# Kernel tuning notes

Hardware: AMD Instinct MI355X
Metric: run time of the kernel (lower is better)

Reference implementation:

```python
import jax, jax.numpy as jnp
from jax import lax
import numpy as np

EPS = 1e-8
NUM_ROUTES = 1152  # 32 * 6 * 6
NUM_OBJ = 10
OBJ_DIM = 16
PC_CAPS = 8
PC_CH = 32


def _squash(s, axis=-1):
    sq = jnp.sum(s * s, axis=axis, keepdims=True)
    return (sq / (1.0 + sq)) * s / jnp.sqrt(sq + EPS)


def setup_inputs() -> dict:
    key = jax.random.key(0)
    ks = jax.random.split(key, 12)
    B = 512
    image = jax.random.uniform(ks[0], (B, 1, 28, 28), dtype=jnp.float32)
    label = jax.random.randint(ks[1], (B,), 0, NUM_OBJ)
    conv_w = jax.random.normal(ks[2], (256, 1, 9, 9), dtype=jnp.float32) * 0.05
    conv_b = jnp.zeros((256,), jnp.float32)
    pc_w = jax.random.normal(ks[3], (PC_CAPS, PC_CH, 256, 9, 9), dtype=jnp.float32) * 0.02
    pc_b = jnp.zeros((PC_CAPS, PC_CH), jnp.float32)
    W_route = jax.random.normal(ks[4], (NUM_ROUTES, NUM_OBJ, OBJ_DIM, PC_CAPS), dtype=jnp.float32)
    dec_w1 = jax.random.normal(ks[5], (512, NUM_OBJ * OBJ_DIM), dtype=jnp.float32) * 0.05
    dec_b1 = jnp.zeros((512,), jnp.float32)
    dec_w2 = jax.random.normal(ks[6], (1024, 512), dtype=jnp.float32) * 0.05
    dec_b2 = jnp.zeros((1024,), jnp.float32)
    dec_w3 = jax.random.normal(ks[7], (784, 1024), dtype=jnp.float32) * 0.05
    dec_b3 = jnp.zeros((784,), jnp.float32)
    return {"image": image, "label": label, "conv_w": conv_w, "conv_b": conv_b,
            "pc_w": pc_w, "pc_b": pc_b, "W_route": W_route,
            "dec_w1": dec_w1, "dec_b1": dec_b1, "dec_w2": dec_w2, "dec_b2": dec_b2,
            "dec_w3": dec_w3, "dec_b3": dec_b3}


def reference(image, label, conv_w, conv_b, pc_w, pc_b, W_route,
              dec_w1, dec_b1, dec_w2, dec_b2, dec_w3, dec_b3):
    B = image.shape[0]
    # ConvEncoder: [B,1,28,28] -> [B,256,20,20]
    x = lax.conv_general_dilated(image, conv_w, (1, 1), 'VALID',
                                 dimension_numbers=('NCHW', 'OIHW', 'NCHW'))
    x = jax.nn.relu(x + conv_b[None, :, None, None])
    # PrimaryCaps: 8 parallel convs fused into one conv with 8*32 out channels
    pw = pc_w.reshape(PC_CAPS * PC_CH, 256, 9, 9)
    u = lax.conv_general_dilated(x, pw, (2, 2), 'VALID',
                                 dimension_numbers=('NCHW', 'OIHW', 'NCHW'))
    u = u + pc_b.reshape(-1)[None, :, None, None]  # [B,256,6,6] == stack dim=1 of [B,8,32,6,6]
    # faithful torch .view: [B,8,32,6,6] row-major -> [B,1152,8]
    u = u.reshape(B, NUM_ROUTES, PC_CAPS)
    u = _squash(u, axis=-1)
    # ObjectCaps dynamic routing
    # u_hat[b,r,j,o] = sum_c W[r,j,o,c] * u[b,r,c]
    u_hat = jnp.einsum('rjoc,brc->brjo', W_route, u)  # [B,1152,10,16]
    b_ij = jnp.zeros((B, NUM_ROUTES, NUM_OBJ), u_hat.dtype)
    v = None
    for it in range(3):
        c_ij = jax.nn.softmax(b_ij, axis=2)                  # softmax over capsules j
        s_j = jnp.einsum('brj,brjo->bjo', c_ij, u_hat)       # [B,10,16]
        v = _squash(s_j, axis=-1)
        if it < 2:
            b_ij = b_ij + jnp.einsum('brjo,bjo->brj', u_hat, v)
    obj_vectors = v[..., None]  # [B,10,16,1]
    # safe_norm over dim=2, squeeze(-1)
    y_prob = jnp.sqrt(jnp.sum(v * v, axis=-1) + EPS)  # [B,10]
    # Decoder: mask by label one-hot, MLP to reconstruction
    mask = jax.nn.one_hot(label, NUM_OBJ, dtype=v.dtype)
    masked = (v * mask[:, :, None]).reshape(B, NUM_OBJ * OBJ_DIM)
    h = jax.nn.relu(masked @ dec_w1.T + dec_b1)
    h = jax.nn.relu(h @ dec_w2.T + dec_b2)
    recon = jax.nn.sigmoid(h @ dec_w3.T + dec_b3).reshape(B, 1, 28, 28)
    return obj_vectors, recon, y_prob
```

## Files before the change

kernel.cpp:

```cpp
#include <hip/hip_runtime.h>
#include <hip/hip_bf16.h>

#define EPSF 1e-8f

typedef __attribute__((ext_vector_type(8))) short short8v;
typedef __attribute__((ext_vector_type(4))) float float4v;

#define XREG 29248
#define XSLOT 7312

static __device__ __forceinline__ unsigned short f2bf_bits(float x)
{
    return __builtin_bit_cast(unsigned short, __float2bfloat16(x));
}

__global__ __launch_bounds__(256) void k_bw2(const float* __restrict__ pw,
                                             __hip_bfloat16* __restrict__ Bw2)
{
    const int oc = blockIdx.x;
    const int t = threadIdx.x;
    __shared__ unsigned short wl[20736];
    for (int i = t; i < 20736; i += 256)
        wl[i] = f2bf_bits(pw[(size_t)oc * 20736 + i]);
    __syncthreads();
    const int r16 = oc & 15, nt = (oc >> 4) & 3, wcq = oc >> 6;
    for (int e = t; e < 2592; e += 256) {
        const int kidx = e >> 5, icc = (e >> 2) & 7, slot = e & 3;
        short8v v;
        #pragma unroll
        for (int i = 0; i < 8; ++i)
            v[i] = (short)wl[(icc * 32 + slot * 8 + i) * 81 + kidx];
        const int chunk = ((kidx * 8 + icc) * 4 + wcq) * 4 + nt;
        *(short8v*)(Bw2 + (size_t)chunk * 512 + (slot * 16 + r16) * 8) = v;
    }
}

__global__ __launch_bounds__(256) void k_conv1(const float* __restrict__ img,
                                               const float* __restrict__ cw,
                                               const float* __restrict__ cb,
                                               __hip_bfloat16* __restrict__ xt)
{
    const int b = blockIdx.x;
    const int c = threadIdx.x;
    __shared__ float simg[784];
    for (int i = c; i < 784; i += 256) simg[i] = img[b * 784 + i];
    float wreg[81];
    const float* wp = cw + c * 81;
    #pragma unroll
    for (int k = 0; k < 81; ++k) wreg[k] = wp[k];
    const float bias = cb[c];
    __syncthreads();

    const int icc = c >> 5, slot = (c >> 3) & 3, ic8 = c & 7;
    char* xbase = (char*)xt + ((size_t)b * 8 + icc) * XREG + slot * XSLOT + ic8 * 2;

    for (int h = 0; h < 20; ++h) {
        for (int wg = 0; wg < 5; ++wg) {
            float acc[4] = {bias, bias, bias, bias};
            #pragma unroll
            for (int ky = 0; ky < 9; ++ky) {
                const float* rp = &simg[(h + ky) * 28 + wg * 4];
                float v[12];
                #pragma unroll
                for (int i = 0; i < 12; ++i) v[i] = rp[i];
                #pragma unroll
                for (int kx = 0; kx < 9; ++kx) {
                    const float wv = wreg[ky * 9 + kx];
                    #pragma unroll
                    for (int i = 0; i < 4; ++i)
                        acc[i] = fmaf(v[kx + i], wv, acc[i]);
                }
            }
            #pragma unroll
            for (int i = 0; i < 4; ++i) {
                int w = wg * 4 + i;
                float av = fmaxf(acc[i], 0.f);
                int pos = 23 * h + 10 * (w & 1) + (w >> 1);
                *(unsigned short*)(xbase + pos * 16) = f2bf_bits(av);
            }
        }
    }
}

__device__ __forceinline__ void stage_x(const __hip_bfloat16* __restrict__ xt,
                                        char* dst, int b0, int icc, int t)
{
    const char* base0 = (const char*)xt + ((size_t)(b0    ) * 8 + icc) * XREG;
    const char* base1 = (const char*)xt + ((size_t)(b0 + 1) * 8 + icc) * XREG;
    #pragma unroll
    for (int k = 0; k < 7; ++k) {
        const int unit = t + k * 512;
        const char* gp = (unit < 1828) ? (base0 + unit * 16)
                                       : (base1 + (unit - 1828) * 16);
        __builtin_amdgcn_global_load_lds(
            (const __attribute__((address_space(1))) unsigned int*)gp,
            (__attribute__((address_space(3))) unsigned int*)(dst + unit * 16),
            16, 0, 0);
    }
    if (t < 72) {
        const int unit = 3584 + t;
        const char* gp = base1 + (unit - 1828) * 16;
        __builtin_amdgcn_global_load_lds(
            (const __attribute__((address_space(1))) unsigned int*)gp,
            (__attribute__((address_space(3))) unsigned int*)(dst + unit * 16),
            16, 0, 0);
    }
}

__global__ __launch_bounds__(512, 1) void k_conv2(const __hip_bfloat16* __restrict__ xt,
                                                  const __hip_bfloat16* __restrict__ Bw2,
                                                  const float* __restrict__ pcb,
                                                  float* __restrict__ u)
{
    const int b0 = blockIdx.x * 2;
    const int t = threadIdx.x;
    const int lane = t & 63, wid = t >> 6;
    const int wr = wid >> 2, wc = wid & 3;
    const int r16 = lane & 15, slot = lane >> 4;

    __shared__ alignas(16) char xs[2][58496];

    int lc[3];
    #pragma unroll
    for (int mt = 0; mt < 3; ++mt) {
        int hw = mt * 16 + r16;
        if (hw >= 36) hw = 0;
        int h = hw / 6, w = hw - h * 6;
        lc[mt] = 46 * h + w;
    }
    const int abase0 = wr * XREG + slot * XSLOT;

    float4v acc[3][4];
    #pragma unroll
    for (int mt = 0; mt < 3; ++mt)
        #pragma unroll
        for (int nt = 0; nt < 4; ++nt)
            acc[mt][nt] = (float4v){0.f, 0.f, 0.f, 0.f};

    stage_x(xt, xs[0], b0, 0, t);
    __syncthreads();

    for (int icc = 0; icc < 8; ++icc) {
        const int cur = icc & 1;
        if (icc < 7) stage_x(xt, xs[cur ^ 1], b0, icc + 1, t);

        const char* xw = xs[cur];
        const __hip_bfloat16* bp = Bw2 + ((size_t)icc * 4 + wc) * 2048 + lane * 8;

        for (int ky = 0; ky < 9; ++ky) {
            const char* ap0 = xw + abase0 + (lc[0] + 23 * ky) * 16;
            const char* ap1 = xw + abase0 + (lc[1] + 23 * ky) * 16;
            const char* ap2 = xw + abase0 + (lc[2] + 23 * ky) * 16;
            const __hip_bfloat16* bk = bp + (size_t)ky * 9 * 65536;
            #pragma unroll
            for (int kx = 0; kx < 9; ++kx) {
                const int C = (10 * (kx & 1) + (kx >> 1)) * 16;
                short8v a0 = *(const short8v*)(ap0 + C);
                short8v a1 = *(const short8v*)(ap1 + C);
                short8v a2 = *(const short8v*)(ap2 + C);
                const __hip_bfloat16* bq = bk + (size_t)kx * 65536;
                short8v bv0 = *(const short8v*)(bq);
                short8v bv1 = *(const short8v*)(bq + 512);
                short8v bv2 = *(const short8v*)(bq + 1024);
                short8v bv3 = *(const short8v*)(bq + 1536);
                acc[0][0] = __builtin_amdgcn_mfma_f32_16x16x32_bf16(a0, bv0, acc[0][0], 0, 0, 0);
                acc[0][1] = __builtin_amdgcn_mfma_f32_16x16x32_bf16(a0, bv1, acc[0][1], 0, 0, 0);
                acc[0][2] = __builtin_amdgcn_mfma_f32_16x16x32_bf16(a0, bv2, acc[0][2], 0, 0, 0);
                acc[0][3] = __builtin_amdgcn_mfma_f32_16x16x32_bf16(a0, bv3, acc[0][3], 0, 0, 0);
                acc[1][0] = __builtin_amdgcn_mfma_f32_16x16x32_bf16(a1, bv0, acc[1][0], 0, 0, 0);
                acc[1][1] = __builtin_amdgcn_mfma_f32_16x16x32_bf16(a1, bv1, acc[1][1], 0, 0, 0);
                acc[1][2] = __builtin_amdgcn_mfma_f32_16x16x32_bf16(a1, bv2, acc[1][2], 0, 0, 0);
                acc[1][3] = __builtin_amdgcn_mfma_f32_16x16x32_bf16(a1, bv3, acc[1][3], 0, 0, 0);
                acc[2][0] = __builtin_amdgcn_mfma_f32_16x16x32_bf16(a2, bv0, acc[2][0], 0, 0, 0);
                acc[2][1] = __builtin_amdgcn_mfma_f32_16x16x32_bf16(a2, bv1, acc[2][1], 0, 0, 0);
                acc[2][2] = __builtin_amdgcn_mfma_f32_16x16x32_bf16(a2, bv2, acc[2][2], 0, 0, 0);
                acc[2][3] = __builtin_amdgcn_mfma_f32_16x16x32_bf16(a2, bv3, acc[2][3], 0, 0, 0);
            }
        }
        __syncthreads();
    }

    const int b = b0 + wr;
    #pragma unroll
    for (int mt = 0; mt < 3; ++mt) {
        int hwb = mt * 16 + slot * 4;
        if (hwb < 36) {
            #pragma unroll
            for (int nt = 0; nt < 4; ++nt) {
                int oc = wc * 64 + nt * 16 + r16;
                float pb = pcb[oc];
                float4v v = acc[mt][nt];
                v.x += pb; v.y += pb; v.z += pb; v.w += pb;
                *(float4v*)(u + (size_t)b * 9216 + oc * 36 + hwb) = v;
            }
        }
    }
}

__global__ void k_squash_u(float* __restrict__ u, int ngroups)
{
    int g = blockIdx.x * blockDim.x + threadIdx.x;
    if (g >= ngroups) return;
    float4v* p = (float4v*)(u + (size_t)g * 8);
    float4v a = p[0], c = p[1];
    float sq = a.x * a.x + a.y * a.y + a.z * a.z + a.w * a.w
             + c.x * c.x + c.y * c.y + c.z * c.z + c.w * c.w;
    float scale = (sq / (1.f + sq)) / sqrtf(sq + EPSF);
    a *= scale; c *= scale;
    p[0] = a; p[1] = c;
}

__global__ __launch_bounds__(256, 2) void k_route3(const float* __restrict__ u,
                                                   const float* __restrict__ W,
                                                   const float* __restrict__ vsum,
                                                   float* __restrict__ spart, int iter)
{
    const int bid = blockIdx.x;
    const int rc = bid % 144;
    const int bc = bid / 144;
    const int r0 = rc * 8;
    const int b0 = bc * 64;
    const int t = threadIdx.x;
    const int oq = t & 3;
    const int img = t >> 2;
    const int b = b0 + img;

    __shared__ alignas(16) float Wl[10240];
    __shared__ alignas(16) float ul[64 * 68];

    #pragma unroll
    for (int k = 0; k < 10; ++k) {
        int e = t + k * 256;
        int rr = e / 320, rest = e - rr * 320;
        float4v val = *(const float4v*)(W + (size_t)(r0 + rr) * 1280 + rest * 4);
        int es = e ^ ((e >> 3) & 3);
        *(float4v*)(Wl + es * 4) = val;
    }
    #pragma unroll
    for (int k = 0; k < 4; ++k) {
        int e = t + k * 256;
        int im = e >> 4, f4 = e & 15;
        float4v val = *(const float4v*)(u + (size_t)(b0 + im) * 9216 + rc * 64 + f4 * 4);
        *(float4v*)(ul + im * 68 + f4 * 4) = val;
    }
    __syncthreads();

    float4v vv[10];
    if (iter > 0) {
        #pragma unroll
        for (int j = 0; j < 10; ++j)
            vv[j] = *(const float4v*)(vsum + (size_t)b * 160 + j * 16 + oq * 4);
    }

    float4v acc[10];
    #pragma unroll
    for (int j = 0; j < 10; ++j) acc[j] = (float4v){0.f, 0.f, 0.f, 0.f};

    const float* up = ul + img * 68;

    for (int r = 0; r < 8; ++r) {
        float4v u0 = *(const float4v*)(up + r * 8);
        float4v u1 = *(const float4v*)(up + r * 8 + 4);
        float4v uh[10];
        #pragma unroll
        for (int j = 0; j < 10; ++j) {
            #pragma unroll
            for (int oo = 0; oo < 4; ++oo) {
                int un = r * 320 + j * 32 + oq * 8 + oo * 2;
                int i0 = un ^ oq;
                int i1 = i0 ^ 1;
                float4v wlo = *(const float4v*)(Wl + i0 * 4);
                float4v whi = *(const float4v*)(Wl + i1 * 4);
                uh[j][oo] = wlo.x * u0.x + wlo.y * u0.y + wlo.z * u0.z + wlo.w * u0.w
                          + whi.x * u1.x + whi.y * u1.y + whi.z * u1.z + whi.w * u1.w;
            }
        }
        if (iter > 0) {
            float q[10];
            #pragma unroll
            for (int j = 0; j < 10; ++j) {
                float qp = uh[j].x * vv[j].x + uh[j].y * vv[j].y
                         + uh[j].z * vv[j].z + uh[j].w * vv[j].w;
                qp += __shfl_xor(qp, 1);
                qp += __shfl_xor(qp, 2);
                q[j] = qp;
            }
            float mx = q[0];
            #pragma unroll
            for (int j = 1; j < 10; ++j) mx = fmaxf(mx, q[j]);
            float ssum = 0.f;
            float c[10];
            #pragma unroll
            for (int j = 0; j < 10; ++j) { c[j] = __expf(q[j] - mx); ssum += c[j]; }
            float inv = 1.f / ssum;
            #pragma unroll
            for (int j = 0; j < 10; ++j) acc[j] += (c[j] * inv) * uh[j];
        } else {
            #pragma unroll
            for (int j = 0; j < 10; ++j) acc[j] += 0.1f * uh[j];
        }
    }

    float* dst = spart + ((size_t)rc * 512 + b) * 160 + oq * 4;
    #pragma unroll
    for (int j = 0; j < 10; ++j)
        *(float4v*)(dst + j * 16) = acc[j];
}

__global__ void k_finish(const float* __restrict__ spart, float* __restrict__ vsum,
                         const int* __restrict__ label, float* __restrict__ obj,
                         float* __restrict__ yprob, float* __restrict__ masked, int iter)
{
    const int b = blockIdx.x, t = threadIdx.x;
    if (t < 160) {
        const float* sp = spart + (size_t)b * 160 + t;
        float sv = 0.f;
        #pragma unroll 8
        for (int rc = 0; rc < 144; ++rc)
            sv += sp[(size_t)rc * 81920];
        float sq = sv * sv;
        sq += __shfl_xor(sq, 1); sq += __shfl_xor(sq, 2);
        sq += __shfl_xor(sq, 4); sq += __shfl_xor(sq, 8);
        float v = sv * (sq / (1.f + sq)) / sqrtf(sq + EPSF);
        float pv = (iter > 0) ? vsum[b * 160 + t] : 0.f;
        vsum[b * 160 + t] = pv + v;
        if (iter == 2) {
            obj[b * 160 + t] = v;
            float vv = v * v;
            vv += __shfl_xor(vv, 1); vv += __shfl_xor(vv, 2);
            vv += __shfl_xor(vv, 4); vv += __shfl_xor(vv, 8);
            int j = t >> 4;
            if ((t & 15) == 0) yprob[b * 10 + j] = sqrtf(vv + EPSF);
            masked[b * 160 + t] = (label[b] == j) ? v : 0.f;
        }
    }
}

__global__ void k_mlp(const float* __restrict__ A, const float* __restrict__ Wt,
                      const float* __restrict__ bias, float* __restrict__ C,
                      int N, int K, int act)
{
    const int m0 = blockIdx.x * 32;
    const int n0 = blockIdx.y * 32;
    const int t  = threadIdx.x;
    const int tn = t & 31, tg = t >> 5;
    __shared__ float As[32][33];
    __shared__ float Ws[32][33];
    float acc[4] = {0.f, 0.f, 0.f, 0.f};
    for (int k0 = 0; k0 < K; k0 += 32) {
        __syncthreads();
        for (int idx = t; idx < 1024; idx += 256) {
            int rr = idx >> 5, kk = idx & 31;
            As[rr][kk] = A[(size_t)(m0 + rr) * K + k0 + kk];
            int n = n0 + rr;
            Ws[rr][kk] = (n < N) ? Wt[(size_t)n * K + k0 + kk] : 0.f;
        }
        __syncthreads();
        #pragma unroll 8
        for (int kk = 0; kk < 32; ++kk) {
            float bv = Ws[tn][kk];
            #pragma unroll
            for (int i = 0; i < 4; ++i)
                acc[i] += As[tg * 4 + i][kk] * bv;
        }
    }
    int n = n0 + tn;
    if (n < N) {
        float bs = bias[n];
        #pragma unroll
        for (int i = 0; i < 4; ++i) {
            float vv = acc[i] + bs;
            vv = (act == 0) ? fmaxf(vv, 0.f) : 1.f / (1.f + expf(-vv));
            C[(size_t)(m0 + tg * 4 + i) * N + n] = vv;
        }
    }
}

extern "C" void kernel_launch(void* const* d_in, const int* in_sizes, int n_in,
                              void* d_out, int out_size, void* d_ws, size_t ws_size,
                              hipStream_t stream)
{
    const float* image  = (const float*)d_in[0];
    const int*   label  = (const int*)  d_in[1];
    const float* conv_w = (const float*)d_in[2];
    const float* conv_b = (const float*)d_in[3];
    const float* pc_w   = (const float*)d_in[4];
    const float* pc_b   = (const float*)d_in[5];
    const float* Wrt    = (const float*)d_in[6];
    const float* dw1 = (const float*)d_in[7];
    const float* db1 = (const float*)d_in[8];
    const float* dw2 = (const float*)d_in[9];
    const float* db2 = (const float*)d_in[10];
    const float* dw3 = (const float*)d_in[11];
    const float* db3 = (const float*)d_in[12];
    float* out = (float*)d_out;

    char* p = (char*)d_ws;
    __hip_bfloat16* xt  = (__hip_bfloat16*)p; p += (size_t)512 * 8 * XREG;
    float* u      = (float*)p; p += 18874368;
    __hip_bfloat16* Bw2 = (__hip_bfloat16*)p; p += 10616832;
    float* vsum   = (float*)p; p += 327680;
    float* masked = (float*)p; p += 327680;
    float* h1     = (float*)p; p += 1048576;
    float* h2     = (float*)p; p += 2097152;

    float* spart = (float*)xt;

    float* obj   = out;
    float* recon = out + 81920;
    float* yprob = out + 483328;

    k_bw2<<<256, 256, 0, stream>>>(pc_w, Bw2);
    k_conv1<<<512, 256, 0, stream>>>(image, conv_w, conv_b, xt);
    k_conv2<<<256, 512, 0, stream>>>(xt, Bw2, pc_b, u);
    k_squash_u<<<2304, 256, 0, stream>>>(u, 589824);
    for (int it = 0; it < 3; ++it) {
        k_route3<<<1152, 256, 0, stream>>>(u, Wrt, vsum, spart, it);
        k_finish<<<512, 192, 0, stream>>>(spart, vsum, label, obj, yprob, masked, it);
    }
    k_mlp<<<dim3(16, 16), 256, 0, stream>>>(masked, dw1, db1, h1, 512, 160, 0);
    k_mlp<<<dim3(16, 32), 256, 0, stream>>>(h1, dw2, db2, h2, 1024, 512, 0);
    k_mlp<<<dim3(16, 25), 256, 0, stream>>>(h2, dw3, db3, recon, 784, 1024, 1);
}
```

Measured before the change: 786.3 us.

## Use one image per conv2 block and software-pipeline A/B fragment loads

The primary-caps conv kernel now has each 256-thread block handle one image instead of two, halving LDS per block so two blocks can share a CU, and the grid grows from 256 to 512 blocks. The 9x9 kernel loop is fully unrolled into a rotating register pipeline that prefetches B weight fragments three steps ahead and A fragments from LDS two steps ahead, to hide global and LDS latency behind the MFMAs. In exchange, each B weight fragment is now fetched by twice as many blocks, and the deeper register buffering raises register pressure under the two-blocks-per-CU launch bound.

```diff
diff --git a/kernel.cpp b/kernel.cpp
--- a/kernel.cpp
+++ b/kernel.cpp
@@ -12,6 +12,11 @@
 static __device__ __forceinline__ unsigned short f2bf_bits(float x)
 {
     return __builtin_bit_cast(unsigned short, __float2bfloat16(x));
+}
+
+__device__ constexpr int aoff(int k)
+{
+    return (23 * (k / 9) + 10 * ((k % 9) & 1) + ((k % 9) >> 1)) * 16;
 }
 
 __global__ __launch_bounds__(256) void k_bw2(const float* __restrict__ pw,
@@ -83,42 +88,37 @@
 }
 
 __device__ __forceinline__ void stage_x(const __hip_bfloat16* __restrict__ xt,
-                                        char* dst, int b0, int icc, int t)
-{
-    const char* base0 = (const char*)xt + ((size_t)(b0    ) * 8 + icc) * XREG;
-    const char* base1 = (const char*)xt + ((size_t)(b0 + 1) * 8 + icc) * XREG;
+                                        char* dst, int b, int icc, int t)
+{
+    const char* base = (const char*)xt + ((size_t)b * 8 + icc) * XREG;
     #pragma unroll
     for (int k = 0; k < 7; ++k) {
-        const int unit = t + k * 512;
-        const char* gp = (unit < 1828) ? (base0 + unit * 16)
-                                       : (base1 + (unit - 1828) * 16);
+        const int unit = t + k * 256;
         __builtin_amdgcn_global_load_lds(
-            (const __attribute__((address_space(1))) unsigned int*)gp,
+            (const __attribute__((address_space(1))) unsigned int*)(base + unit * 16),
             (__attribute__((address_space(3))) unsigned int*)(dst + unit * 16),
             16, 0, 0);
     }
-    if (t < 72) {
-        const int unit = 3584 + t;
-        const char* gp = base1 + (unit - 1828) * 16;
+    if (t < 36) {
+        const int unit = 1792 + t;
         __builtin_amdgcn_global_load_lds(
-            (const __attribute__((address_space(1))) unsigned int*)gp,
+            (const __attribute__((address_space(1))) unsigned int*)(base + unit * 16),
             (__attribute__((address_space(3))) unsigned int*)(dst + unit * 16),
             16, 0, 0);
     }
 }
 
-__global__ __launch_bounds__(512, 1) void k_conv2(const __hip_bfloat16* __restrict__ xt,
+__global__ __launch_bounds__(256, 2) void k_conv2(const __hip_bfloat16* __restrict__ xt,
                                                   const __hip_bfloat16* __restrict__ Bw2,
                                                   const float* __restrict__ pcb,
                                                   float* __restrict__ u)
 {
-    const int b0 = blockIdx.x * 2;
+    const int b = blockIdx.x;
     const int t = threadIdx.x;
-    const int lane = t & 63, wid = t >> 6;
-    const int wr = wid >> 2, wc = wid & 3;
+    const int lane = t & 63, wc = t >> 6;
     const int r16 = lane & 15, slot = lane >> 4;
 
-    __shared__ alignas(16) char xs[2][58496];
+    __shared__ alignas(16) char xs[2][29248];
 
     int lc[3];
     #pragma unroll
@@ -128,7 +128,7 @@
         int h = hw / 6, w = hw - h * 6;
         lc[mt] = 46 * h + w;
     }
-    const int abase0 = wr * XREG + slot * XSLOT;
+    const int abase0 = slot * XSLOT;
 
     float4v acc[3][4];
     #pragma unroll
@@ -137,50 +137,69 @@
         for (int nt = 0; nt < 4; ++nt)
             acc[mt][nt] = (float4v){0.f, 0.f, 0.f, 0.f};
 
-    stage_x(xt, xs[0], b0, 0, t);
+    stage_x(xt, xs[0], b, 0, t);
     __syncthreads();
 
     for (int icc = 0; icc < 8; ++icc) {
         const int cur = icc & 1;
-        if (icc < 7) stage_x(xt, xs[cur ^ 1], b0, icc + 1, t);
+        if (icc < 7) stage_x(xt, xs[cur ^ 1], b, icc + 1, t);
 
         const char* xw = xs[cur];
+        const char* apm0 = xw + abase0 + lc[0] * 16;
+        const char* apm1 = xw + abase0 + lc[1] * 16;
+        const char* apm2 = xw + abase0 + lc[2] * 16;
         const __hip_bfloat16* bp = Bw2 + ((size_t)icc * 4 + wc) * 2048 + lane * 8;
 
+        short8v a[3][3];
+        short8v bv[4][4];
+        #pragma unroll
+        for (int pk = 0; pk < 2; ++pk) {
+            const int off = aoff(pk);
+            a[pk][0] = *(const short8v*)(apm0 + off);
+            a[pk][1] = *(const short8v*)(apm1 + off);
+            a[pk][2] = *(const short8v*)(apm2 + off);
+        }
+        #pragma unroll
+        for (int pk = 0; pk < 3; ++pk) {
+            const __hip_bfloat16* bq = bp + (size_t)pk * 65536;
+            bv[pk][0] = *(const short8v*)(bq);
+            bv[pk][1] = *(const short8v*)(bq + 512);
+            bv[pk][2] = *(const short8v*)(bq + 1024);
+            bv[pk][3] = *(const short8v*)(bq + 1536);
+        }
+
+        #pragma unroll
         for (int ky = 0; ky < 9; ++ky) {
-            const char* ap0 = xw + abase0 + (lc[0] + 23 * ky) * 16;
-            const char* ap1 = xw + abase0 + (lc[1] + 23 * ky) * 16;
-            const char* ap2 = xw + abase0 + (lc[2] + 23 * ky) * 16;
-            const __hip_bfloat16* bk = bp + (size_t)ky * 9 * 65536;
             #pragma unroll
             for (int kx = 0; kx < 9; ++kx) {
-                const int C = (10 * (kx & 1) + (kx >> 1)) * 16;
-                short8v a0 = *(const short8v*)(ap0 + C);
-                short8v a1 = *(const short8v*)(ap1 + C);
-                short8v a2 = *(const short8v*)(ap2 + C);
-                const __hip_bfloat16* bq = bk + (size_t)kx * 65536;
-                short8v bv0 = *(const short8v*)(bq);
-                short8v bv1 = *(const short8v*)(bq + 512);
-                short8v bv2 = *(const short8v*)(bq + 1024);
-                short8v bv3 = *(const short8v*)(bq + 1536);
-                acc[0][0] = __builtin_amdgcn_mfma_f32_16x16x32_bf16(a0, bv0, acc[0][0], 0, 0, 0);
-                acc[0][1] = __builtin_amdgcn_mfma_f32_16x16x32_bf16(a0, bv1, acc[0][1], 0, 0, 0);
-                acc[0][2] = __builtin_amdgcn_mfma_f32_16x16x32_bf16(a0, bv2, acc[0][2], 0, 0, 0);
-                acc[0][3] = __builtin_amdgcn_mfma_f32_16x16x32_bf16(a0, bv3, acc[0][3], 0, 0, 0);
-                acc[1][0] = __builtin_amdgcn_mfma_f32_16x16x32_bf16(a1, bv0, acc[1][0], 0, 0, 0);
-                acc[1][1] = __builtin_amdgcn_mfma_f32_16x16x32_bf16(a1, bv1, acc[1][1], 0, 0, 0);
-                acc[1][2] = __builtin_amdgcn_mfma_f32_16x16x32_bf16(a1, bv2, acc[1][2], 0, 0, 0);
-                acc[1][3] = __builtin_amdgcn_mfma_f32_16x16x32_bf16(a1, bv3, acc[1][3], 0, 0, 0);
-                acc[2][0] = __builtin_amdgcn_mfma_f32_16x16x32_bf16(a2, bv0, acc[2][0], 0, 0, 0);
-                acc[2][1] = __builtin_amdgcn_mfma_f32_16x16x32_bf16(a2, bv1, acc[2][1], 0, 0, 0);
-                acc[2][2] = __builtin_amdgcn_mfma_f32_16x16x32_bf16(a2, bv2, acc[2][2], 0, 0, 0);
-                acc[2][3] = __builtin_amdgcn_mfma_f32_16x16x32_bf16(a2, bv3, acc[2][3], 0, 0, 0);
+                const int k = ky * 9 + kx;
+                const int ca = k % 3, cb = k & 3;
+                if (k + 3 <= 80) {
+                    const int pb3 = (k + 3) & 3;
+                    const __hip_bfloat16* bq = bp + (size_t)(k + 3) * 65536;
+                    bv[pb3][0] = *(const short8v*)(bq);
+                    bv[pb3][1] = *(const short8v*)(bq + 512);
+                    bv[pb3][2] = *(const short8v*)(bq + 1024);
+                    bv[pb3][3] = *(const short8v*)(bq + 1536);
+                }
+                if (k + 2 <= 80) {
+                    const int pa2 = (k + 2) % 3;
+                    const int off = aoff(k + 2);
+                    a[pa2][0] = *(const short8v*)(apm0 + off);
+                    a[pa2][1] = *(const short8v*)(apm1 + off);
+                    a[pa2][2] = *(const short8v*)(apm2 + off);
+                }
+                #pragma unroll
+                for (int mt = 0; mt < 3; ++mt)
+                    #pragma unroll
+                    for (int nt = 0; nt < 4; ++nt)
+                        acc[mt][nt] = __builtin_amdgcn_mfma_f32_16x16x32_bf16(
+                            a[ca][mt], bv[cb][nt], acc[mt][nt], 0, 0, 0);
             }
         }
         __syncthreads();
     }
 
-    const int b = b0 + wr;
     #pragma unroll
     for (int mt = 0; mt < 3; ++mt) {
         int hwb = mt * 16 + slot * 4;
@@ -412,7 +431,7 @@
 
     k_bw2<<<256, 256, 0, stream>>>(pc_w, Bw2);
     k_conv1<<<512, 256, 0, stream>>>(image, conv_w, conv_b, xt);
-    k_conv2<<<256, 512, 0, stream>>>(xt, Bw2, pc_b, u);
+    k_conv2<<<512, 256, 0, stream>>>(xt, Bw2, pc_b, u);
     k_squash_u<<<2304, 256, 0, stream>>>(u, 589824);
     for (int it = 0; it < 3; ++it) {
         k_route3<<<1152, 256, 0, stream>>>(u, Wrt, vsum, spart, it);
```

New measurement: 795.3 us. No clear change (+1.1%).

## Retile primary-caps conv to four images by half output channels

Applied to the files above, without the earlier changes.

Each conv2 block now covers four images and half of the output channels (two warps per image, two column groups), where before it covered two images and all channels. Each weight fragment loaded from global is now reused across four images instead of two, halving weight traffic per image. In exchange the LDS double buffer is dropped for a single buffer with two barriers per input-channel chunk, so staging no longer overlaps compute, and the input activations are loaded twice (once per channel half).

```diff
diff --git a/kernel.cpp b/kernel.cpp
--- a/kernel.cpp
+++ b/kernel.cpp
@@ -82,27 +82,26 @@
     }
 }
 
-__device__ __forceinline__ void stage_x(const __hip_bfloat16* __restrict__ xt,
-                                        char* dst, int b0, int icc, int t)
-{
-    const char* base0 = (const char*)xt + ((size_t)(b0    ) * 8 + icc) * XREG;
-    const char* base1 = (const char*)xt + ((size_t)(b0 + 1) * 8 + icc) * XREG;
-    #pragma unroll
-    for (int k = 0; k < 7; ++k) {
-        const int unit = t + k * 512;
-        const char* gp = (unit < 1828) ? (base0 + unit * 16)
-                                       : (base1 + (unit - 1828) * 16);
+__device__ __forceinline__ void stage_x4(const __hip_bfloat16* __restrict__ xt,
+                                         char* dst, int b0, int icc, int t)
+{
+    #pragma unroll
+    for (int k = 0; k < 14; ++k) {
+        const int e = t + k * 512;
+        const int im = e / 1828, unit = e - im * 1828;
+        const char* gp = (const char*)xt + ((size_t)(b0 + im) * 8 + icc) * XREG + unit * 16;
         __builtin_amdgcn_global_load_lds(
             (const __attribute__((address_space(1))) unsigned int*)gp,
-            (__attribute__((address_space(3))) unsigned int*)(dst + unit * 16),
+            (__attribute__((address_space(3))) unsigned int*)(dst + e * 16),
             16, 0, 0);
     }
-    if (t < 72) {
-        const int unit = 3584 + t;
-        const char* gp = base1 + (unit - 1828) * 16;
+    if (t < 144) {
+        const int e = 7168 + t;
+        const int im = e / 1828, unit = e - im * 1828;
+        const char* gp = (const char*)xt + ((size_t)(b0 + im) * 8 + icc) * XREG + unit * 16;
         __builtin_amdgcn_global_load_lds(
             (const __attribute__((address_space(1))) unsigned int*)gp,
-            (__attribute__((address_space(3))) unsigned int*)(dst + unit * 16),
+            (__attribute__((address_space(3))) unsigned int*)(dst + e * 16),
             16, 0, 0);
     }
 }
@@ -112,13 +111,16 @@
                                                   const float* __restrict__ pcb,
                                                   float* __restrict__ u)
 {
-    const int b0 = blockIdx.x * 2;
+    const int quad = blockIdx.x >> 1;
+    const int ochalf = blockIdx.x & 1;
+    const int b0 = quad * 4;
     const int t = threadIdx.x;
     const int lane = t & 63, wid = t >> 6;
-    const int wr = wid >> 2, wc = wid & 3;
+    const int wr = wid >> 1, wc = wid & 1;
+    const int WC = ochalf * 2 + wc;
     const int r16 = lane & 15, slot = lane >> 4;
 
-    __shared__ alignas(16) char xs[2][58496];
+    __shared__ alignas(16) char xs[4 * 29248];
 
     int lc[3];
     #pragma unroll
@@ -137,24 +139,23 @@
         for (int nt = 0; nt < 4; ++nt)
             acc[mt][nt] = (float4v){0.f, 0.f, 0.f, 0.f};
 
-    stage_x(xt, xs[0], b0, 0, t);
-    __syncthreads();
-
     for (int icc = 0; icc < 8; ++icc) {
-        const int cur = icc & 1;
-        if (icc < 7) stage_x(xt, xs[cur ^ 1], b0, icc + 1, t);
-
-        const char* xw = xs[cur];
-        const __hip_bfloat16* bp = Bw2 + ((size_t)icc * 4 + wc) * 2048 + lane * 8;
+        __syncthreads();
+        stage_x4(xt, xs, b0, icc, t);
+        __syncthreads();
+
+        const char* xw = xs;
+        const char* ap0 = xw + abase0 + lc[0] * 16;
+        const char* ap1 = xw + abase0 + lc[1] * 16;
+        const char* ap2 = xw + abase0 + lc[2] * 16;
+        const __hip_bfloat16* bp = Bw2 + ((size_t)icc * 4 + WC) * 2048 + lane * 8;
 
         for (int ky = 0; ky < 9; ++ky) {
-            const char* ap0 = xw + abase0 + (lc[0] + 23 * ky) * 16;
-            const char* ap1 = xw + abase0 + (lc[1] + 23 * ky) * 16;
-            const char* ap2 = xw + abase0 + (lc[2] + 23 * ky) * 16;
+            const int rb = (23 * ky) * 16;
             const __hip_bfloat16* bk = bp + (size_t)ky * 9 * 65536;
             #pragma unroll
             for (int kx = 0; kx < 9; ++kx) {
-                const int C = (10 * (kx & 1) + (kx >> 1)) * 16;
+                const int C = rb + (10 * (kx & 1) + (kx >> 1)) * 16;
                 short8v a0 = *(const short8v*)(ap0 + C);
                 short8v a1 = *(const short8v*)(ap1 + C);
                 short8v a2 = *(const short8v*)(ap2 + C);
@@ -177,7 +178,6 @@
                 acc[2][3] = __builtin_amdgcn_mfma_f32_16x16x32_bf16(a2, bv3, acc[2][3], 0, 0, 0);
             }
         }
-        __syncthreads();
     }
 
     const int b = b0 + wr;
@@ -187,7 +187,7 @@
         if (hwb < 36) {
             #pragma unroll
             for (int nt = 0; nt < 4; ++nt) {
-                int oc = wc * 64 + nt * 16 + r16;
+                int oc = ochalf * 128 + wc * 64 + nt * 16 + r16;
                 float pb = pcb[oc];
                 float4v v = acc[mt][nt];
                 v.x += pb; v.y += pb; v.z += pb; v.w += pb;
```

Result: faster. 769.5 us (-2.1%).
